# Kernel tuning notes

Hardware: AMD Instinct MI355X
Metric: run time of the kernel (lower is better)

The kernel has to match this reference:

```python
import jax, jax.numpy as jnp
import numpy as np

LN_EPS = 1e-5


def _ln_all_nonbatch(t):
    # torch nn.LayerNorm(t.size()[1:]) created fresh each call: identity affine,
    # normalize jointly over all non-batch dims, biased variance, eps=1e-5.
    axes = tuple(range(1, t.ndim))
    mu = jnp.mean(t, axis=axes, keepdims=True)
    var = jnp.mean(jnp.square(t - mu), axis=axes, keepdims=True)
    return (t - mu) / jnp.sqrt(var + LN_EPS)


def setup_inputs() -> dict:
    key = jax.random.key(0)
    kx, kq, kk, kv = jax.random.split(key, 4)
    B, S, E, d = 32, 1024, 768, 64
    x = jax.random.normal(kx, (B, S, E), dtype=jnp.float32)
    Wq = jax.random.normal(kq, (E, d), dtype=jnp.float32)
    Wk = jax.random.normal(kk, (E, d), dtype=jnp.float32)
    Wv = jax.random.normal(kv, (E, d), dtype=jnp.float32)
    return {"x": x, "Wq": Wq, "Wk": Wk, "Wv": Wv}


def reference(x, Wq, Wk, Wv):
    # x: [B,S,E]; Wq/Wk/Wv: [E,d]
    Q = jnp.einsum('bse,ed->bsd', x, Wq)            # [B,S,d]
    K = jnp.swapaxes(jnp.einsum('bse,ed->bsd', x, Wk), -2, -1)  # [B,d,S]
    V = jnp.einsum('bse,ed->bsd', x, Wv)            # [B,S,d]
    Q = _ln_all_nonbatch(Q)
    K = _ln_all_nonbatch(K)
    V = _ln_all_nonbatch(V)
    d = Q.shape[-1]  # K.shape[1] after transpose == head dim
    scores = jnp.einsum('bsd,bdt->bst', Q, K) / jnp.sqrt(jnp.float32(d))  # [B,S,S]
    attn = jax.nn.softmax(scores, axis=-1)
    return jnp.einsum('bst,btd->bsd', attn, V)      # [B,S,d]
```

## Files before the change

kernel.cpp:

```cpp
#include <hip/hip_runtime.h>
#include <hip/hip_fp16.h>

typedef _Float16 f16x8 __attribute__((ext_vector_type(8)));
typedef _Float16 f16x4 __attribute__((ext_vector_type(4)));
typedef float    f32x4 __attribute__((ext_vector_type(4)));

#define NB   32
#define SEQ  1024
#define EDIM 768
#define HD   64
#define MTOT (NB * SEQ)
#define LOG2E 1.44269504088896340736f

__device__ __forceinline__ void barrier_lgkm_only() {
    __builtin_amdgcn_sched_barrier(0);
    asm volatile("s_waitcnt lgkmcnt(0)" ::: "memory");
    __builtin_amdgcn_sched_barrier(0);
    __builtin_amdgcn_s_barrier();
    __builtin_amdgcn_sched_barrier(0);
}

__global__ __launch_bounds__(256) void pack_w(const float* __restrict__ Wq,
                                              const float* __restrict__ Wk,
                                              const float* __restrict__ Wv,
                                              _Float16* __restrict__ Wt) {
    int c = blockIdx.x;
    const float* src = (c < 64) ? Wq : (c < 128) ? Wk : Wv;
    int cc = c & 63;
    for (int e = threadIdx.x; e < EDIM; e += 256)
        Wt[(size_t)c * EDIM + e] = (_Float16)src[(size_t)e * HD + cc];
}

#define PROJ_STEP(T, XN, WN, XW, WW)                                                   \
  {                                                                                    \
    if ((T) <= 9) {                               \
      const int e0 = ((T) + 2) * 64;                                                   \
      _Pragma("unroll")                                                                \
      for (int i = 0; i < 4; ++i) {                                                    \
        int lin = tid + i * 256, r = lin >> 4, c4 = (lin & 15) * 4;                    \
        XN[i] = *(const f32x4*)&x[(size_t)(m0 + r) * EDIM + e0 + c4];                  \
      }                                                                                \
      _Pragma("unroll")                                                                \
      for (int i = 0; i < 6; ++i) {                                                    \
        int lin = tid + i * 256, c = lin >> 3, c8 = (lin & 7) * 8;                     \
        WN[i] = *(const f16x8*)&Wt[(size_t)c * EDIM + e0 + c8];                        \
      }                                                                                \
    }                                                                                  \
    {                                                      \
      const int cur = (T) & 1;                                                         \
      f16x8 af[4][2];                                                                  \
      _Pragma("unroll")                                                                \
      for (int rg = 0; rg < 4; ++rg) {                                                 \
        af[rg][0] = *(const f16x8*)&xs[cur][rg * 16 + lr][lk];                         \
        af[rg][1] = *(const f16x8*)&xs[cur][rg * 16 + lr][32 + lk];                    \
      }                                                                                \
      _Pragma("unroll")                                                                \
      for (int c = 0; c < 3; ++c) {                                                    \
        const int nb = wave * 3 + c;                                                   \
        f16x8 b0 = *(const f16x8*)&wsh[cur][nb * 16 + lr][lk];                         \
        f16x8 b1 = *(const f16x8*)&wsh[cur][nb * 16 + lr][32 + lk];                    \
        _Pragma("unroll")                                                              \
        for (int rg = 0; rg < 4; ++rg) {                                               \
          acc[rg][c] = __builtin_amdgcn_mfma_f32_16x16x32_f16(af[rg][0], b0, acc[rg][c], 0, 0, 0); \
          acc[rg][c] = __builtin_amdgcn_mfma_f32_16x16x32_f16(af[rg][1], b1, acc[rg][c], 0, 0, 0); \
        }                                                                              \
      }                                                                                \
    }                                                                                  \
    if ((T) <= 10) {   \
      const int nxt = ((T) + 1) & 1;                                                   \
      _Pragma("unroll")                                                                \
      for (int i = 0; i < 4; ++i) {                                                    \
        int lin = tid + i * 256, r = lin >> 4, c4 = (lin & 15) * 4;                    \
        f16x4 h;                                                                       \
        h[0] = (_Float16)XW[i][0]; h[1] = (_Float16)XW[i][1];                          \
        h[2] = (_Float16)XW[i][2]; h[3] = (_Float16)XW[i][3];                          \
        *(f16x4*)&xs[nxt][r][c4] = h;                                                  \
      }                                                                                \
      _Pragma("unroll")                                                                \
      for (int i = 0; i < 6; ++i) {                                                    \
        int lin = tid + i * 256, c = lin >> 3, c8 = (lin & 7) * 8;                     \
        *(f16x8*)&wsh[nxt][c][c8] = WW[i];                                             \
      }                                                                                \
      barrier_lgkm_only();                                                             \
    }                                                                                  \
  }

__global__ __launch_bounds__(256, 2) void proj_kernel(const float* __restrict__ x,
                                                      const _Float16* __restrict__ Wt,
                                                      _Float16* __restrict__ q16,
                                                      _Float16* __restrict__ k16,
                                                      _Float16* __restrict__ v16t,
                                                      float* __restrict__ part,
                                                      float* __restrict__ ksum) {
    __shared__ _Float16 xs[2][64][72];
    __shared__ _Float16 wsh[2][192][72];
    __shared__ float red[4][6];
    __shared__ float kred[2][64];
    const int tid = threadIdx.x, wave = tid >> 6, lane = tid & 63;
    const int lr = lane & 15, lk = (lane >> 4) * 8, lrow = (lane >> 4) * 4;
    const int m0 = blockIdx.x * 64;
    const int bb = m0 >> 10;

    f32x4 acc[4][3] = {};
    f32x4 xv0[4], xv1[4];
    f16x8 wv0[6], wv1[6];

    #pragma unroll
    for (int i = 0; i < 4; ++i) {
        int lin = tid + i * 256, r = lin >> 4, c4 = (lin & 15) * 4;
        xv0[i] = *(const f32x4*)&x[(size_t)(m0 + r) * EDIM + c4];
    }
    #pragma unroll
    for (int i = 0; i < 6; ++i) {
        int lin = tid + i * 256, c = lin >> 3, c8 = (lin & 7) * 8;
        wv0[i] = *(const f16x8*)&Wt[(size_t)c * EDIM + c8];
    }
    #pragma unroll
    for (int i = 0; i < 4; ++i) {
        int lin = tid + i * 256, r = lin >> 4, c4 = (lin & 15) * 4;
        f16x4 h;
        h[0] = (_Float16)xv0[i][0]; h[1] = (_Float16)xv0[i][1];
        h[2] = (_Float16)xv0[i][2]; h[3] = (_Float16)xv0[i][3];
        *(f16x4*)&xs[0][r][c4] = h;
    }
    #pragma unroll
    for (int i = 0; i < 6; ++i) {
        int lin = tid + i * 256, c = lin >> 3, c8 = (lin & 7) * 8;
        *(f16x8*)&wsh[0][c][c8] = wv0[i];
    }
    #pragma unroll
    for (int i = 0; i < 4; ++i) {
        int lin = tid + i * 256, r = lin >> 4, c4 = (lin & 15) * 4;
        xv1[i] = *(const f32x4*)&x[(size_t)(m0 + r) * EDIM + 64 + c4];
    }
    #pragma unroll
    for (int i = 0; i < 6; ++i) {
        int lin = tid + i * 256, c = lin >> 3, c8 = (lin & 7) * 8;
        wv1[i] = *(const f16x8*)&Wt[(size_t)c * EDIM + 64 + c8];
    }
    barrier_lgkm_only();

    PROJ_STEP(0,  xv0, wv0, xv1, wv1)
    PROJ_STEP(1,  xv1, wv1, xv0, wv0)
    PROJ_STEP(2,  xv0, wv0, xv1, wv1)
    PROJ_STEP(3,  xv1, wv1, xv0, wv0)
    PROJ_STEP(4,  xv0, wv0, xv1, wv1)
    PROJ_STEP(5,  xv1, wv1, xv0, wv0)
    PROJ_STEP(6,  xv0, wv0, xv1, wv1)
    PROJ_STEP(7,  xv1, wv1, xv0, wv0)
    PROJ_STEP(8,  xv0, wv0, xv1, wv1)
    PROJ_STEP(9,  xv1, wv1, xv0, wv0)
    PROJ_STEP(10, xv0, wv0, xv1, wv1)
    PROJ_STEP(11, xv1, wv1, xv0, wv0)

    #pragma unroll
    for (int rg = 0; rg < 4; ++rg) {
        const int rbase = m0 + rg * 16 + lrow;
        const int rowin = (m0 & 1023) + rg * 16 + lrow;
        #pragma unroll
        for (int c = 0; c < 3; ++c) {
            const int nb = wave * 3 + c;
            if (nb < 8) {
                _Float16* dst = (nb < 4) ? q16 : k16;
                int lc = (nb & 3) * 16 + lr;
                #pragma unroll
                for (int j = 0; j < 4; ++j)
                    dst[(size_t)(rbase + j) * HD + lc] = (_Float16)acc[rg][c][j];
            } else {
                int col = (nb & 3) * 16 + lr;
                f16x4 h;
                #pragma unroll
                for (int j = 0; j < 4; ++j) h[j] = (_Float16)acc[rg][c][j];
                *(f16x4*)&v16t[((size_t)(bb * 64 + col)) * SEQ + rowin] = h;
            }
        }
    }

    if (wave == 1 || wave == 2) {
        #pragma unroll
        for (int rg = 0; rg < 4; ++rg) {
            #pragma unroll
            for (int j = 0; j < 4; ++j) {
                float ks = (wave == 1) ? (acc[rg][1][j] + acc[rg][2][j])
                                       : (acc[rg][0][j] + acc[rg][1][j]);
                ks += __shfl_xor(ks, 1); ks += __shfl_xor(ks, 2);
                ks += __shfl_xor(ks, 4); ks += __shfl_xor(ks, 8);
                if (lr == 0) kred[wave - 1][rg * 16 + lrow + j] = ks;
            }
        }
    }

    float sq = 0.f, qq = 0.f, sk = 0.f, qk = 0.f, sv = 0.f, qv = 0.f;
    #pragma unroll
    for (int c = 0; c < 3; ++c) {
        const int nb = wave * 3 + c;
        float s = 0.f, q = 0.f;
        #pragma unroll
        for (int rg = 0; rg < 4; ++rg)
            #pragma unroll
            for (int j = 0; j < 4; ++j) { float v = acc[rg][c][j]; s += v; q += v * v; }
        if (nb < 4)      { sq += s; qq += q; }
        else if (nb < 8) { sk += s; qk += q; }
        else             { sv += s; qv += q; }
    }
    #pragma unroll
    for (int off = 1; off < 64; off <<= 1) {
        sq += __shfl_xor(sq, off); qq += __shfl_xor(qq, off);
        sk += __shfl_xor(sk, off); qk += __shfl_xor(qk, off);
        sv += __shfl_xor(sv, off); qv += __shfl_xor(qv, off);
    }
    if (lane == 0) {
        red[wave][0] = sq; red[wave][1] = qq;
        red[wave][2] = sk; red[wave][3] = qk;
        red[wave][4] = sv; red[wave][5] = qv;
    }
    __syncthreads();
    if (tid < 64) ksum[m0 + tid] = kred[0][tid] + kred[1][tid];
    if (tid < 6)
        part[blockIdx.x * 6 + tid] = red[0][tid] + red[1][tid] + red[2][tid] + red[3][tid];
}

__global__ __launch_bounds__(64) void stats_reduce(const float* __restrict__ part,
                                                   float* __restrict__ stats) {
    int b = blockIdx.x, a = threadIdx.x;
    if (a < 3) {
        double s = 0.0, q = 0.0;
        for (int i = 0; i < 16; ++i) {
            s += (double)part[(b * 16 + i) * 6 + a * 2];
            q += (double)part[(b * 16 + i) * 6 + a * 2 + 1];
        }
        double mean = s / 65536.0;
        double var  = q / 65536.0 - mean * mean;
        stats[b * 8 + a * 2 + 0] = (float)mean;
        stats[b * 8 + a * 2 + 1] = (float)(1.0 / sqrt(var + 1e-5));
    }
}

__global__ __launch_bounds__(256) void attn_kernel(const _Float16* __restrict__ q16,
                                                   const _Float16* __restrict__ k16,
                                                   const _Float16* __restrict__ v16t,
                                                   const float* __restrict__ stats,
                                                   const float* __restrict__ ksum,
                                                   float* __restrict__ out) {
    __shared__ _Float16 ksm[64][72];
    __shared__ _Float16 vsm[64][72];
    __shared__ _Float16 psm[4][16][72];
    const int d_ = blockIdx.x;
    const int b = (d_ & 7) * 4 + ((d_ >> 3) & 3), qt = d_ >> 5;
    const int tid = threadIdx.x, wave = tid >> 6, lane = tid & 63;
    const int lr = lane & 15, lk = (lane >> 4) * 8, lrow = (lane >> 4) * 4;
    const float sscale = stats[b * 8 + 1] * stats[b * 8 + 3] * 0.125f * LOG2E;
    const float adjscale = sscale * stats[b * 8 + 0];
    const float mv = stats[b * 8 + 4], rv = stats[b * 8 + 5];
    const int q0 = qt * 64 + wave * 16;
    const _Float16* Qb = q16 + ((size_t)b * SEQ + q0) * HD;
    const float* ksb = ksum + b * SEQ;

    f16x8 aq0 = *(const f16x8*)&Qb[(size_t)lr * HD + lk];
    f16x8 aq1 = *(const f16x8*)&Qb[(size_t)lr * HD + 32 + lk];

    f32x4 o[4] = {};
    float mrow[4], lsum[4];
    #pragma unroll
    for (int j = 0; j < 4; ++j) { mrow[j] = -1e30f; lsum[j] = 0.f; }

    for (int kv0 = 0; kv0 < SEQ; kv0 += 64) {
        for (int i = 0; i < 2; ++i) {
            int lin = tid + i * 256;
            int r = lin >> 3, c = (lin & 7) * 8;
            *(f16x8*)&ksm[r][c] = *(const f16x8*)&k16[((size_t)b * SEQ + kv0 + r) * HD + c];
        }
        for (int i = 0; i < 2; ++i) {
            int lin = tid + i * 256;
            int dd = lin >> 3, c = (lin & 7) * 8;
            *(f16x8*)&vsm[dd][c] = *(const f16x8*)&v16t[((size_t)b * HD + dd) * SEQ + kv0 + c];
        }
        __syncthreads();

        f32x4 sa[4];
        float adjv[4];
        #pragma unroll
        for (int cb = 0; cb < 4; ++cb) {
            sa[cb] = (f32x4){0.f, 0.f, 0.f, 0.f};
            f16x8 bk0 = *(const f16x8*)&ksm[cb * 16 + lr][lk];
            f16x8 bk1 = *(const f16x8*)&ksm[cb * 16 + lr][32 + lk];
            sa[cb] = __builtin_amdgcn_mfma_f32_16x16x32_f16(aq0, bk0, sa[cb], 0, 0, 0);
            sa[cb] = __builtin_amdgcn_mfma_f32_16x16x32_f16(aq1, bk1, sa[cb], 0, 0, 0);
            adjv[cb] = adjscale * ksb[kv0 + cb * 16 + lr];
        }

        #pragma unroll
        for (int j = 0; j < 4; ++j) {
            float sv0 = sa[0][j] * sscale - adjv[0];
            float sv1 = sa[1][j] * sscale - adjv[1];
            float sv2 = sa[2][j] * sscale - adjv[2];
            float sv3 = sa[3][j] * sscale - adjv[3];
            float pm = fmaxf(fmaxf(sv0, sv1), fmaxf(sv2, sv3));
            pm = fmaxf(pm, __shfl_xor(pm, 1));
            pm = fmaxf(pm, __shfl_xor(pm, 2));
            pm = fmaxf(pm, __shfl_xor(pm, 4));
            pm = fmaxf(pm, __shfl_xor(pm, 8));
            float mnew  = fmaxf(mrow[j], pm);
            float alpha = exp2f(mrow[j] - mnew);
            mrow[j] = mnew;
            float p0 = exp2f(sv0 - mnew), p1 = exp2f(sv1 - mnew);
            float p2 = exp2f(sv2 - mnew), p3 = exp2f(sv3 - mnew);
            sa[0][j] = p0; sa[1][j] = p1; sa[2][j] = p2; sa[3][j] = p3;
            float rs = (p0 + p1) + (p2 + p3);
            rs += __shfl_xor(rs, 1); rs += __shfl_xor(rs, 2);
            rs += __shfl_xor(rs, 4); rs += __shfl_xor(rs, 8);
            lsum[j] = lsum[j] * alpha + rs;
            o[0][j] *= alpha; o[1][j] *= alpha; o[2][j] *= alpha; o[3][j] *= alpha;
        }
        #pragma unroll
        for (int cb = 0; cb < 4; ++cb)
            #pragma unroll
            for (int j = 0; j < 4; ++j)
                psm[wave][lrow + j][cb * 16 + lr] = (_Float16)sa[cb][j];

        f16x8 pa0 = *(const f16x8*)&psm[wave][lr][lk];
        f16x8 pa1 = *(const f16x8*)&psm[wave][lr][32 + lk];
        #pragma unroll
        for (int db = 0; db < 4; ++db) {
            f16x8 bv0 = *(const f16x8*)&vsm[db * 16 + lr][lk];
            f16x8 bv1 = *(const f16x8*)&vsm[db * 16 + lr][32 + lk];
            o[db] = __builtin_amdgcn_mfma_f32_16x16x32_f16(pa0, bv0, o[db], 0, 0, 0);
            o[db] = __builtin_amdgcn_mfma_f32_16x16x32_f16(pa1, bv1, o[db], 0, 0, 0);
        }
        __syncthreads();
    }

    #pragma unroll
    for (int j = 0; j < 4; ++j) {
        float inv = 1.f / lsum[j];
        size_t row = (size_t)b * SEQ + q0 + lrow + j;
        #pragma unroll
        for (int db = 0; db < 4; ++db)
            out[row * HD + db * 16 + lr] = rv * (o[db][j] * inv - mv);
    }
}

extern "C" void kernel_launch(void* const* d_in, const int* in_sizes, int n_in,
                              void* d_out, int out_size, void* d_ws, size_t ws_size,
                              hipStream_t stream) {
    const float* x  = (const float*)d_in[0];
    const float* Wq = (const float*)d_in[1];
    const float* Wk = (const float*)d_in[2];
    const float* Wv = (const float*)d_in[3];
    float* out = (float*)d_out;
    char* ws = (char*)d_ws;

    _Float16* Wt   = (_Float16*)ws;
    float* stats   = (float*)(ws + 0x50000);
    float* ksum    = (float*)(ws + 0x51000);
    float* part    = (float*)(ws + 0x72000);
    _Float16* q16  = (_Float16*)(ws + 0x100000);
    _Float16* k16  = (_Float16*)(ws + 0x500000);
    _Float16* v16t = (_Float16*)(ws + 0x900000);

    pack_w<<<192, 256, 0, stream>>>(Wq, Wk, Wv, Wt);
    proj_kernel<<<MTOT / 64, 256, 0, stream>>>(x, Wt, q16, k16, v16t, part, ksum);
    stats_reduce<<<NB, 64, 0, stream>>>(part, stats);
    attn_kernel<<<NB * 16, 256, 0, stream>>>(q16, k16, v16t, stats, ksum, out);
}
```

Before: 73.30 us.

## Load projection weights directly into registers and halve row tile per block

The projection kernel no longer stages the fp16 weight tile through shared memory. Each wave loads its B fragments straight from global memory into registers, double-buffered across k-steps. The row tile per block drops from 64 to 32, so twice as many blocks launch, and the occupancy hint rises to 3 blocks per CU; the stats reduction now sums 32 partials per batch instead of 16. This removes the weight LDS writes and reads plus most of the LDS footprint, at the cost of redundant global and L2 reads of the weights across more blocks and fewer MFMAs per weight fragment.

```diff
diff --git a/kernel.cpp b/kernel.cpp
--- a/kernel.cpp
+++ b/kernel.cpp
@@ -31,130 +31,97 @@
         Wt[(size_t)c * EDIM + e] = (_Float16)src[(size_t)e * HD + cc];
 }
 
-#define PROJ_STEP(T, XN, WN, XW, WW)                                                   \
+#define LOADB(DST, KT)                                                                 \
+    _Pragma("unroll")                                                                  \
+    for (int c = 0; c < 3; ++c) {                                                      \
+        const int nb = wave * 3 + c;                                                   \
+        DST[c * 2]     = *(const f16x8*)&Wt[(size_t)(nb * 16 + lr) * EDIM + (KT) * 64 + lk]; \
+        DST[c * 2 + 1] = *(const f16x8*)&Wt[(size_t)(nb * 16 + lr) * EDIM + (KT) * 64 + 32 + lk]; \
+    }
+
+#define LOADX(DST, KT)                                                                 \
+    _Pragma("unroll")                                                                  \
+    for (int i = 0; i < 2; ++i) {                                                      \
+        int lin = tid + i * 256, r = lin >> 4, c4 = (lin & 15) * 4;                    \
+        DST[i] = *(const f32x4*)&x[(size_t)(m0 + r) * EDIM + (KT) * 64 + c4];          \
+    }
+
+#define STAGEX(SRC, B)                                                                 \
+    _Pragma("unroll")                                                                  \
+    for (int i = 0; i < 2; ++i) {                                                      \
+        int lin = tid + i * 256, r = lin >> 4, c4 = (lin & 15) * 4;                    \
+        f16x4 h;                                                                       \
+        h[0] = (_Float16)SRC[i][0]; h[1] = (_Float16)SRC[i][1];                        \
+        h[2] = (_Float16)SRC[i][2]; h[3] = (_Float16)SRC[i][3];                        \
+        *(f16x4*)&xs[B][r][c4] = h;                                                    \
+    }
+
+#define PROJ_STEP(T, BC, BN, XN, XW)                                                   \
   {                                                                                    \
-    if ((T) <= 9) {                               \
-      const int e0 = ((T) + 2) * 64;                                                   \
+    if ((T) <= 10) { LOADB(BN, (T) + 1) }    \
+    if ((T) <= 9)  { LOADX(XN, (T) + 2) }                   \
+    {                                                                                  \
+      const int cur = (T) & 1;                                                         \
+      f16x8 af[2][2];                                                                  \
       _Pragma("unroll")                                                                \
-      for (int i = 0; i < 4; ++i) {                                                    \
-        int lin = tid + i * 256, r = lin >> 4, c4 = (lin & 15) * 4;                    \
-        XN[i] = *(const f32x4*)&x[(size_t)(m0 + r) * EDIM + e0 + c4];                  \
-      }                                                                                \
-      _Pragma("unroll")                                                                \
-      for (int i = 0; i < 6; ++i) {                                                    \
-        int lin = tid + i * 256, c = lin >> 3, c8 = (lin & 7) * 8;                     \
-        WN[i] = *(const f16x8*)&Wt[(size_t)c * EDIM + e0 + c8];                        \
-      }                                                                                \
-    }                                                                                  \
-    {                                                      \
-      const int cur = (T) & 1;                                                         \
-      f16x8 af[4][2];                                                                  \
-      _Pragma("unroll")                                                                \
-      for (int rg = 0; rg < 4; ++rg) {                                                 \
+      for (int rg = 0; rg < 2; ++rg) {                                                 \
         af[rg][0] = *(const f16x8*)&xs[cur][rg * 16 + lr][lk];                         \
         af[rg][1] = *(const f16x8*)&xs[cur][rg * 16 + lr][32 + lk];                    \
       }                                                                                \
       _Pragma("unroll")                                                                \
-      for (int c = 0; c < 3; ++c) {                                                    \
-        const int nb = wave * 3 + c;                                                   \
-        f16x8 b0 = *(const f16x8*)&wsh[cur][nb * 16 + lr][lk];                         \
-        f16x8 b1 = *(const f16x8*)&wsh[cur][nb * 16 + lr][32 + lk];                    \
+      for (int c = 0; c < 3; ++c)                                                      \
         _Pragma("unroll")                                                              \
-        for (int rg = 0; rg < 4; ++rg) {                                               \
-          acc[rg][c] = __builtin_amdgcn_mfma_f32_16x16x32_f16(af[rg][0], b0, acc[rg][c], 0, 0, 0); \
-          acc[rg][c] = __builtin_amdgcn_mfma_f32_16x16x32_f16(af[rg][1], b1, acc[rg][c], 0, 0, 0); \
+        for (int rg = 0; rg < 2; ++rg) {                                               \
+          acc[rg][c] = __builtin_amdgcn_mfma_f32_16x16x32_f16(af[rg][0], BC[c * 2],     acc[rg][c], 0, 0, 0); \
+          acc[rg][c] = __builtin_amdgcn_mfma_f32_16x16x32_f16(af[rg][1], BC[c * 2 + 1], acc[rg][c], 0, 0, 0); \
         }                                                                              \
-      }                                                                                \
     }                                                                                  \
-    if ((T) <= 10) {   \
-      const int nxt = ((T) + 1) & 1;                                                   \
-      _Pragma("unroll")                                                                \
-      for (int i = 0; i < 4; ++i) {                                                    \
-        int lin = tid + i * 256, r = lin >> 4, c4 = (lin & 15) * 4;                    \
-        f16x4 h;                                                                       \
-        h[0] = (_Float16)XW[i][0]; h[1] = (_Float16)XW[i][1];                          \
-        h[2] = (_Float16)XW[i][2]; h[3] = (_Float16)XW[i][3];                          \
-        *(f16x4*)&xs[nxt][r][c4] = h;                                                  \
-      }                                                                                \
-      _Pragma("unroll")                                                                \
-      for (int i = 0; i < 6; ++i) {                                                    \
-        int lin = tid + i * 256, c = lin >> 3, c8 = (lin & 7) * 8;                     \
-        *(f16x8*)&wsh[nxt][c][c8] = WW[i];                                             \
-      }                                                                                \
+    if ((T) <= 10) {                                                                   \
+      STAGEX(XW, ((T) + 1) & 1)                                                        \
       barrier_lgkm_only();                                                             \
     }                                                                                  \
   }
 
-__global__ __launch_bounds__(256, 2) void proj_kernel(const float* __restrict__ x,
+__global__ __launch_bounds__(256, 3) void proj_kernel(const float* __restrict__ x,
                                                       const _Float16* __restrict__ Wt,
                                                       _Float16* __restrict__ q16,
                                                       _Float16* __restrict__ k16,
                                                       _Float16* __restrict__ v16t,
                                                       float* __restrict__ part,
                                                       float* __restrict__ ksum) {
-    __shared__ _Float16 xs[2][64][72];
-    __shared__ _Float16 wsh[2][192][72];
+    __shared__ _Float16 xs[2][32][72];
     __shared__ float red[4][6];
-    __shared__ float kred[2][64];
+    __shared__ float kred[2][32];
     const int tid = threadIdx.x, wave = tid >> 6, lane = tid & 63;
     const int lr = lane & 15, lk = (lane >> 4) * 8, lrow = (lane >> 4) * 4;
-    const int m0 = blockIdx.x * 64;
+    const int m0 = blockIdx.x * 32;
     const int bb = m0 >> 10;
 
-    f32x4 acc[4][3] = {};
-    f32x4 xv0[4], xv1[4];
-    f16x8 wv0[6], wv1[6];
-
-    #pragma unroll
-    for (int i = 0; i < 4; ++i) {
-        int lin = tid + i * 256, r = lin >> 4, c4 = (lin & 15) * 4;
-        xv0[i] = *(const f32x4*)&x[(size_t)(m0 + r) * EDIM + c4];
-    }
-    #pragma unroll
-    for (int i = 0; i < 6; ++i) {
-        int lin = tid + i * 256, c = lin >> 3, c8 = (lin & 7) * 8;
-        wv0[i] = *(const f16x8*)&Wt[(size_t)c * EDIM + c8];
-    }
-    #pragma unroll
-    for (int i = 0; i < 4; ++i) {
-        int lin = tid + i * 256, r = lin >> 4, c4 = (lin & 15) * 4;
-        f16x4 h;
-        h[0] = (_Float16)xv0[i][0]; h[1] = (_Float16)xv0[i][1];
-        h[2] = (_Float16)xv0[i][2]; h[3] = (_Float16)xv0[i][3];
-        *(f16x4*)&xs[0][r][c4] = h;
-    }
-    #pragma unroll
-    for (int i = 0; i < 6; ++i) {
-        int lin = tid + i * 256, c = lin >> 3, c8 = (lin & 7) * 8;
-        *(f16x8*)&wsh[0][c][c8] = wv0[i];
-    }
-    #pragma unroll
-    for (int i = 0; i < 4; ++i) {
-        int lin = tid + i * 256, r = lin >> 4, c4 = (lin & 15) * 4;
-        xv1[i] = *(const f32x4*)&x[(size_t)(m0 + r) * EDIM + 64 + c4];
-    }
-    #pragma unroll
-    for (int i = 0; i < 6; ++i) {
-        int lin = tid + i * 256, c = lin >> 3, c8 = (lin & 7) * 8;
-        wv1[i] = *(const f16x8*)&Wt[(size_t)c * EDIM + 64 + c8];
-    }
+    f32x4 acc[2][3] = {};
+    f32x4 xvA[2], xvB[2];
+    f16x8 bA[6], bB[6];
+
+    LOADB(bA, 0)
+    LOADX(xvA, 0)
+    STAGEX(xvA, 0)
+    LOADX(xvB, 1)
     barrier_lgkm_only();
 
-    PROJ_STEP(0,  xv0, wv0, xv1, wv1)
-    PROJ_STEP(1,  xv1, wv1, xv0, wv0)
-    PROJ_STEP(2,  xv0, wv0, xv1, wv1)
-    PROJ_STEP(3,  xv1, wv1, xv0, wv0)
-    PROJ_STEP(4,  xv0, wv0, xv1, wv1)
-    PROJ_STEP(5,  xv1, wv1, xv0, wv0)
-    PROJ_STEP(6,  xv0, wv0, xv1, wv1)
-    PROJ_STEP(7,  xv1, wv1, xv0, wv0)
-    PROJ_STEP(8,  xv0, wv0, xv1, wv1)
-    PROJ_STEP(9,  xv1, wv1, xv0, wv0)
-    PROJ_STEP(10, xv0, wv0, xv1, wv1)
-    PROJ_STEP(11, xv1, wv1, xv0, wv0)
-
-    #pragma unroll
-    for (int rg = 0; rg < 4; ++rg) {
+    PROJ_STEP(0,  bA, bB, xvA, xvB)
+    PROJ_STEP(1,  bB, bA, xvB, xvA)
+    PROJ_STEP(2,  bA, bB, xvA, xvB)
+    PROJ_STEP(3,  bB, bA, xvB, xvA)
+    PROJ_STEP(4,  bA, bB, xvA, xvB)
+    PROJ_STEP(5,  bB, bA, xvB, xvA)
+    PROJ_STEP(6,  bA, bB, xvA, xvB)
+    PROJ_STEP(7,  bB, bA, xvB, xvA)
+    PROJ_STEP(8,  bA, bB, xvA, xvB)
+    PROJ_STEP(9,  bB, bA, xvB, xvA)
+    PROJ_STEP(10, bA, bB, xvA, xvB)
+    PROJ_STEP(11, bB, bA, xvB, xvA)
+
+    #pragma unroll
+    for (int rg = 0; rg < 2; ++rg) {
         const int rbase = m0 + rg * 16 + lrow;
         const int rowin = (m0 & 1023) + rg * 16 + lrow;
         #pragma unroll
@@ -178,7 +145,7 @@
 
     if (wave == 1 || wave == 2) {
         #pragma unroll
-        for (int rg = 0; rg < 4; ++rg) {
+        for (int rg = 0; rg < 2; ++rg) {
             #pragma unroll
             for (int j = 0; j < 4; ++j) {
                 float ks = (wave == 1) ? (acc[rg][1][j] + acc[rg][2][j])
@@ -196,7 +163,7 @@
         const int nb = wave * 3 + c;
         float s = 0.f, q = 0.f;
         #pragma unroll
-        for (int rg = 0; rg < 4; ++rg)
+        for (int rg = 0; rg < 2; ++rg)
             #pragma unroll
             for (int j = 0; j < 4; ++j) { float v = acc[rg][c][j]; s += v; q += v * v; }
         if (nb < 4)      { sq += s; qq += q; }
@@ -215,7 +182,7 @@
         red[wave][4] = sv; red[wave][5] = qv;
     }
     __syncthreads();
-    if (tid < 64) ksum[m0 + tid] = kred[0][tid] + kred[1][tid];
+    if (tid < 32) ksum[m0 + tid] = kred[0][tid] + kred[1][tid];
     if (tid < 6)
         part[blockIdx.x * 6 + tid] = red[0][tid] + red[1][tid] + red[2][tid] + red[3][tid];
 }
@@ -225,9 +192,9 @@
     int b = blockIdx.x, a = threadIdx.x;
     if (a < 3) {
         double s = 0.0, q = 0.0;
-        for (int i = 0; i < 16; ++i) {
-            s += (double)part[(b * 16 + i) * 6 + a * 2];
-            q += (double)part[(b * 16 + i) * 6 + a * 2 + 1];
+        for (int i = 0; i < 32; ++i) {
+            s += (double)part[(b * 32 + i) * 6 + a * 2];
+            q += (double)part[(b * 32 + i) * 6 + a * 2 + 1];
         }
         double mean = s / 65536.0;
         double var  = q / 65536.0 - mean * mean;
@@ -359,7 +326,7 @@
     _Float16* v16t = (_Float16*)(ws + 0x900000);
 
     pack_w<<<192, 256, 0, stream>>>(Wq, Wk, Wv, Wt);
-    proj_kernel<<<MTOT / 64, 256, 0, stream>>>(x, Wt, q16, k16, v16t, part, ksum);
+    proj_kernel<<<MTOT / 32, 256, 0, stream>>>(x, Wt, q16, k16, v16t, part, ksum);
     stats_reduce<<<NB, 64, 0, stream>>>(part, stats);
     attn_kernel<<<NB * 16, 256, 0, stream>>>(q16, k16, v16t, stats, ksum, out);
 }
```

Measured after the change: 89.83 us. +22.5%, slower.
